# Optimization experiments

Hardware: AMD Instinct MI355X
Metric: run time of the kernel (lower is better)

The kernel has to match this reference:

```python
import jax, jax.numpy as jnp
import numpy as np

NUM_HEADS = 16
MASK_NEG = -66504.0  # matches IPEX causal mask fill value


def setup_inputs() -> dict:
    key = jax.random.key(0)
    ks = jax.random.split(key, 5)
    B, S, E = 1, 2048, 2048
    return {
        "hidden_states": jax.random.normal(ks[0], (B, S, E), dtype=jnp.float32),
        "q_wei": jax.random.normal(ks[1], (E, E), dtype=jnp.float32) * (E ** -0.5),
        "k_wei": jax.random.normal(ks[2], (E, E), dtype=jnp.float32) * (E ** -0.5),
        "v_wei": jax.random.normal(ks[3], (E, E), dtype=jnp.float32) * (E ** -0.5),
        "out_wei": jax.random.normal(ks[4], (E, E), dtype=jnp.float32) * (E ** -0.5),
    }


def reference(hidden_states, q_wei, k_wei, v_wei, out_wei):
    B, S, E = hidden_states.shape
    H = NUM_HEADS
    D = E // H
    # qkv_normal (row-major path): x @ W, [B,S,E]
    q = hidden_states @ q_wei
    k = hidden_states @ k_wei
    v = hidden_states @ v_wei
    # compute_qkv view + normal_combine permute -> [B,H,S,D]
    q = q.reshape(B, S, H, D).transpose(0, 2, 1, 3)
    k = k.reshape(B, S, H, D).transpose(0, 2, 1, 3)
    v = v.reshape(B, S, H, D).transpose(0, 2, 1, 3)
    # naive_self_attention: scores, causal mask add, THEN scale divide
    scores = jnp.einsum("bhqd,bhkd->bhqk", q, k)  # [B,H,S,S]
    causal = jnp.triu(jnp.full((S, S), MASK_NEG, dtype=scores.dtype), k=1)
    scores = scores + causal[None, None]
    scores = scores / jnp.sqrt(jnp.asarray(D, dtype=scores.dtype))
    probs = jax.nn.softmax(scores.astype(jnp.float32), axis=-1).astype(q.dtype)
    attn = jnp.einsum("bhqk,bhkd->bhqd", probs, v)  # [B,H,S,D]
    # merge heads and output projection
    attn = attn.transpose(0, 2, 1, 3).reshape(B, S, E)
    return attn @ out_wei
```

## Files before the change

kernel.cpp:

```cpp
#include <hip/hip_runtime.h>

#define F16 _Float16
typedef __attribute__((ext_vector_type(8))) _Float16 half8;
typedef __attribute__((ext_vector_type(4))) float f32x4;

constexpr int S = 2048;
constexpr int E = 2048;
constexpr float MASK_NEG = -66504.0f;
constexpr float INV_SQRT_D = 0.08838834764831845f;
constexpr float MASK_SC = MASK_NEG * INV_SQRT_D;

__device__ __forceinline__ void gload16(const void* g, void* l) {
  __builtin_amdgcn_global_load_lds((const __attribute__((address_space(1))) void*)g,
                                   (__attribute__((address_space(3))) void*)l, 16, 0, 0);
}

__global__ __launch_bounds__(256) void cast_f32_f16_k(const float* __restrict__ x,
                                                      F16* __restrict__ y) {
  size_t i = ((size_t)blockIdx.x * 256 + threadIdx.x) * 8;
  float4 a = *(const float4*)(x + i);
  float4 b = *(const float4*)(x + i + 4);
  half8 h;
  h[0] = (F16)a.x; h[1] = (F16)a.y; h[2] = (F16)a.z; h[3] = (F16)a.w;
  h[4] = (F16)b.x; h[5] = (F16)b.y; h[6] = (F16)b.z; h[7] = (F16)b.w;
  *(half8*)(y + i) = h;
}

__global__ __launch_bounds__(256) void transpose_cast2_k(const float* __restrict__ W0,
                                                         const float* __restrict__ W1,
                                                         F16* __restrict__ D0,
                                                         F16* __restrict__ D1) {
  const float* W = blockIdx.z ? W1 : W0;
  F16* Wt = blockIdx.z ? D1 : D0;
  __shared__ float tile[64][65];
  const int t = threadIdx.x;
  const int bx = blockIdx.x, by = blockIdx.y;
  {
    int r = t >> 4, c = (t & 15) << 2;
    const float* src = W + (size_t)(by * 64 + r) * E + bx * 64 + c;
    #pragma unroll
    for (int i = 0; i < 4; ++i) {
      float4 v = *(const float4*)(src + (size_t)i * 16 * E);
      tile[r + i * 16][c + 0] = v.x; tile[r + i * 16][c + 1] = v.y;
      tile[r + i * 16][c + 2] = v.z; tile[r + i * 16][c + 3] = v.w;
    }
  }
  __syncthreads();
  {
    int r = t >> 2, c = (t & 3) << 4;
    half8 v0, v1;
    #pragma unroll
    for (int i = 0; i < 8; ++i) v0[i] = (F16)tile[c + i][r];
    #pragma unroll
    for (int i = 0; i < 8; ++i) v1[i] = (F16)tile[c + 8 + i][r];
    F16* dst = Wt + (size_t)(bx * 64 + r) * E + by * 64 + c;
    *(half8*)dst = v0;
    *(half8*)(dst + 8) = v1;
  }
}

template <int MODE>
__global__ __launch_bounds__(256, 2) void gemm_bt_k(const F16* __restrict__ A,
                                                    const F16* __restrict__ Bt,
                                                    void* __restrict__ C0v,
                                                    void* __restrict__ C1v) {
  constexpr int K = 2048, N = 2048;
  __shared__ F16 sA[64 * 64];
  __shared__ F16 sB[128 * 64];
  const int t = threadIdx.x;
  const int lane = t & 63, wave = t >> 6;
  const int wr = wave >> 1, wc = wave & 1;
  const int bm = blockIdx.y, bn = blockIdx.x;

  f32x4 acc[2][4];
  #pragma unroll
  for (int mi = 0; mi < 2; ++mi)
    #pragma unroll
    for (int ni = 0; ni < 4; ++ni) acc[mi][ni] = (f32x4){0.f, 0.f, 0.f, 0.f};

  const int rb = t >> 3;
  const int bofs = (t & 7) << 4;
  const int kOff = (bofs ^ ((rb & 7) << 4)) >> 1;
  const F16* aSrc = A + (size_t)(bm * 64 + rb) * K + kOff;
  const F16* bSrc = Bt + (size_t)(bn * 128 + rb) * K + kOff;
  F16* aDst = sA + t * 8;
  F16* bDst = sB + t * 8;

  for (int bk = 0; bk < K; bk += 64) {
    #pragma unroll
    for (int it = 0; it < 2; ++it)
      gload16(aSrc + (size_t)it * 32 * K + bk, aDst + it * 2048);
    #pragma unroll
    for (int it = 0; it < 4; ++it)
      gload16(bSrc + (size_t)it * 32 * K + bk, bDst + it * 2048);
    __syncthreads();
    #pragma unroll
    for (int kk = 0; kk < 2; ++kk) {
      half8 af[2], bf[4];
      const int kb = kk * 64 + ((lane >> 4) << 4);
      #pragma unroll
      for (int i = 0; i < 2; ++i) {
        const int ra = wr * 32 + i * 16 + (lane & 15);
        af[i] = *(const half8*)((const char*)sA + ra * 128 + (kb ^ ((ra & 7) << 4)));
      }
      #pragma unroll
      for (int i = 0; i < 4; ++i) {
        const int rn = wc * 64 + i * 16 + (lane & 15);
        bf[i] = *(const half8*)((const char*)sB + rn * 128 + (kb ^ ((rn & 7) << 4)));
      }
      #pragma unroll
      for (int mi = 0; mi < 2; ++mi)
        #pragma unroll
        for (int ni = 0; ni < 4; ++ni)
          acc[mi][ni] = __builtin_amdgcn_mfma_f32_16x16x32_f16(af[mi], bf[ni], acc[mi][ni], 0, 0, 0);
    }
    __syncthreads();
  }

  const float scale = (MODE == 1 && bn < 16) ? INV_SQRT_D : 1.0f;
  void* Cv = (MODE == 1 && bn >= 16) ? C1v : C0v;
  const int cb = (MODE == 1 ? (bn & 15) : bn) * 128;

  #pragma unroll
  for (int mi = 0; mi < 2; ++mi) {
    const int r0 = bm * 64 + wr * 32 + mi * 16 + ((lane >> 4) << 2);
    #pragma unroll
    for (int ni = 0; ni < 4; ++ni) {
      const int c = cb + wc * 64 + ni * 16 + (lane & 15);
      #pragma unroll
      for (int j = 0; j < 4; ++j) {
        if (MODE == 2)
          ((float*)Cv)[(size_t)(r0 + j) * N + c] = acc[mi][ni][j];
        else
          ((F16*)Cv)[(size_t)(r0 + j) * N + c] = (F16)(acc[mi][ni][j] * scale);
      }
    }
  }
}

__global__ __launch_bounds__(256, 2) void attn_fwd_k(const F16* __restrict__ Q,
                                                     const F16* __restrict__ Km,
                                                     const F16* __restrict__ Vt,
                                                     F16* __restrict__ O) {
  __shared__ F16 sK[2][64 * 128];
  __shared__ F16 sV[2][128 * 64];
  __shared__ F16 sP[4][16 * 64];
  const int t = threadIdx.x, lane = t & 63, w = t >> 6;
  const int h = blockIdx.x & 15;
  const int bq = blockIdx.x >> 4;
  const int qt = (bq < 16) ? (31 - bq) : (bq - 16);
  const int qrow0 = qt * 64 + w * 16;

  half8 qf[4];
  {
    const int r = qrow0 + (lane & 15);
    const F16* qp = Q + (size_t)r * E + h * 128 + ((lane >> 4) << 3);
    #pragma unroll
    for (int kd = 0; kd < 4; ++kd) qf[kd] = *(const half8*)(qp + kd * 32);
  }

  f32x4 oacc[8];
  #pragma unroll
  for (int i = 0; i < 8; ++i) oacc[i] = (f32x4){0.f, 0.f, 0.f, 0.f};
  float mrow[4] = {-3e38f, -3e38f, -3e38f, -3e38f};
  float lrow[4] = {0.f, 0.f, 0.f, 0.f};

  const int rk = t >> 4;
  const int kcol = (((t & 15) << 4) ^ ((rk & 15) << 4)) >> 1;
  const int rv = t >> 3;
  const int vcol = (((t & 7) << 4) ^ ((rv & 7) << 4)) >> 1;
  const F16* kBase = Km + (size_t)rk * E + h * 128 + kcol;
  const F16* vBase = Vt + (size_t)(h * 128 + rv) * S + vcol;
  F16* myP = (F16*)sP[w];

  auto stage = [&](int kt, int b) {
    const F16* kSrc = kBase + (size_t)kt * 64 * E;
    const F16* vSrc = vBase + kt * 64;
    #pragma unroll
    for (int it = 0; it < 4; ++it) {
      gload16(kSrc + (size_t)it * 16 * E, &sK[b][t * 8 + it * 2048]);
      gload16(vSrc + (size_t)it * 32 * S, &sV[b][t * 8 + it * 2048]);
    }
  };

  stage(0, 0);
  const int nt = qt + 1;

  for (int kt = 0; kt < nt; ++kt) {
    __syncthreads();
    if (kt + 1 < nt) stage(kt + 1, (kt + 1) & 1);
    const char* bK = (const char*)sK[kt & 1];
    const char* bV = (const char*)sV[kt & 1];

    f32x4 sacc[4];
    #pragma unroll
    for (int i = 0; i < 4; ++i) sacc[i] = (f32x4){0.f, 0.f, 0.f, 0.f};
    __builtin_amdgcn_s_setprio(1);
    #pragma unroll
    for (int kd = 0; kd < 4; ++kd) {
      const int kb = kd * 64 + ((lane >> 4) << 4);
      #pragma unroll
      for (int ni = 0; ni < 4; ++ni) {
        const int rn = ni * 16 + (lane & 15);
        half8 bf = *(const half8*)(bK + rn * 256 + (kb ^ ((rn & 15) << 4)));
        sacc[ni] = __builtin_amdgcn_mfma_f32_16x16x32_f16(qf[kd], bf, sacc[ni], 0, 0, 0);
      }
    }
    __builtin_amdgcn_s_setprio(0);

    const bool diag = (kt == nt - 1);
    const int qg0 = qrow0 + ((lane >> 4) << 2);
    const int kg0 = kt * 64 + (lane & 15);
    float mxs[4];
    bool need = false;
    #pragma unroll
    for (int j = 0; j < 4; ++j) {
      float mx = -3e38f;
      #pragma unroll
      for (int ni = 0; ni < 4; ++ni) {
        float s = sacc[ni][j];
        if (diag && (kg0 + ni * 16) > (qg0 + j)) s += MASK_SC;
        sacc[ni][j] = s;
        mx = fmaxf(mx, s);
      }
      mx = fmaxf(mx, __shfl_xor(mx, 1));
      mx = fmaxf(mx, __shfl_xor(mx, 2));
      mx = fmaxf(mx, __shfl_xor(mx, 4));
      mx = fmaxf(mx, __shfl_xor(mx, 8));
      mxs[j] = mx;
      need = need || (mx > mrow[j] + 8.0f);
    }
    if (__any(need)) {
      #pragma unroll
      for (int j = 0; j < 4; ++j) {
        const float mnew = fmaxf(mrow[j], mxs[j]);
        const float sc = __expf(mrow[j] - mnew);
        float rs = 0.f;
        #pragma unroll
        for (int ni = 0; ni < 4; ++ni) {
          const float p = __expf(sacc[ni][j] - mnew);
          sacc[ni][j] = p;
          rs += p;
        }
        rs += __shfl_xor(rs, 1);
        rs += __shfl_xor(rs, 2);
        rs += __shfl_xor(rs, 4);
        rs += __shfl_xor(rs, 8);
        lrow[j] = lrow[j] * sc + rs;
        mrow[j] = mnew;
        #pragma unroll
        for (int df = 0; df < 8; ++df) oacc[df][j] *= sc;
      }
    } else {
      #pragma unroll
      for (int j = 0; j < 4; ++j) {
        float rs = 0.f;
        #pragma unroll
        for (int ni = 0; ni < 4; ++ni) {
          const float p = __expf(sacc[ni][j] - mrow[j]);
          sacc[ni][j] = p;
          rs += p;
        }
        rs += __shfl_xor(rs, 1);
        rs += __shfl_xor(rs, 2);
        rs += __shfl_xor(rs, 4);
        rs += __shfl_xor(rs, 8);
        lrow[j] += rs;
      }
    }

    {
      const int rl0 = (lane >> 4) << 2;
      #pragma unroll
      for (int ni = 0; ni < 4; ++ni) {
        const int cb = (ni * 16 + (lane & 15)) * 2;
        #pragma unroll
        for (int j = 0; j < 4; ++j) {
          const int r = rl0 + j;
          *(F16*)((char*)myP + r * 128 + (cb ^ ((r & 7) << 4))) = (F16)sacc[ni][j];
        }
      }
    }

    __builtin_amdgcn_s_setprio(1);
    #pragma unroll
    for (int kk = 0; kk < 2; ++kk) {
      const int kb = kk * 64 + ((lane >> 4) << 4);
      const int ra = lane & 15;
      half8 pa = *(const half8*)((const char*)myP + ra * 128 + (kb ^ ((ra & 7) << 4)));
      #pragma unroll
      for (int df = 0; df < 8; ++df) {
        const int rd = df * 16 + (lane & 15);
        half8 vf = *(const half8*)(bV + rd * 128 + (kb ^ ((rd & 7) << 4)));
        oacc[df] = __builtin_amdgcn_mfma_f32_16x16x32_f16(pa, vf, oacc[df], 0, 0, 0);
      }
    }
    __builtin_amdgcn_s_setprio(0);
  }

  #pragma unroll
  for (int j = 0; j < 4; ++j) {
    const float inv = 1.0f / lrow[j];
    const int r = qrow0 + ((lane >> 4) << 2) + j;
    F16* op = O + (size_t)r * E + h * 128 + (lane & 15);
    #pragma unroll
    for (int df = 0; df < 8; ++df) op[df * 16] = (F16)(oacc[df][j] * inv);
  }
}

extern "C" void kernel_launch(void* const* d_in, const int* in_sizes, int n_in,
                              void* d_out, int out_size, void* d_ws, size_t ws_size,
                              hipStream_t stream) {
  const float* X  = (const float*)d_in[0];
  const float* Wq = (const float*)d_in[1];
  const float* Wk = (const float*)d_in[2];
  const float* Wv = (const float*)d_in[3];
  const float* Wo = (const float*)d_in[4];
  float* out = (float*)d_out;

  const size_t MAT = (size_t)2048 * 2048;
  F16* Xh  = (F16*)d_ws;
  F16* Wt0 = Xh + MAT;
  F16* Wt1 = Wt0 + MAT;
  F16* Qh  = Wt1 + MAT;
  F16* Kh  = Qh + MAT;
  F16* Vh  = Kh + MAT;

  dim3 b256(256);
  cast_f32_f16_k<<<dim3(MAT / 2048), b256, 0, stream>>>(X, Xh);

  transpose_cast2_k<<<dim3(32, 32, 2), b256, 0, stream>>>(Wq, Wk, Wt0, Wt1);
  gemm_bt_k<1><<<dim3(32, 32), b256, 0, stream>>>(Xh, Wt0, Qh, Kh);

  transpose_cast2_k<<<dim3(32, 32, 2), b256, 0, stream>>>(Wv, Wo, Wt0, Wt1);
  gemm_bt_k<0><<<dim3(16, 32), b256, 0, stream>>>(Wt0, Xh, Vh, nullptr);

  attn_fwd_k<<<dim3(512), b256, 0, stream>>>(Qh, Kh, Vh, Xh);

  gemm_bt_k<2><<<dim3(16, 32), b256, 0, stream>>>(Xh, Wt1, out, nullptr);
}
```

Before: 195.1 us.

## Transpose attention MFMA operands so each lane owns one query row

Swaps the A/B operands of both MFMAs in the attention kernel so that S^T and O^T accumulate with each lane holding a single query row. Softmax max and sum reductions drop from four 4-step shuffles per row to two shuffles across lane groups, and running max/sum collapse to one scalar per lane. P is written to shared memory as packed half4 instead of scalar halves, and output stores become half4 vectors. This reduces shuffle and scalar LDS/global store overhead, but changes the register layout and the masking index math.

```diff
diff --git a/kernel.cpp b/kernel.cpp
--- a/kernel.cpp
+++ b/kernel.cpp
@@ -2,6 +2,7 @@
 
 #define F16 _Float16
 typedef __attribute__((ext_vector_type(8))) _Float16 half8;
+typedef __attribute__((ext_vector_type(4))) _Float16 half4;
 typedef __attribute__((ext_vector_type(4))) float f32x4;
 
 constexpr int S = 2048;
@@ -150,11 +151,12 @@
   const int bq = blockIdx.x >> 4;
   const int qt = (bq < 16) ? (31 - bq) : (bq - 16);
   const int qrow0 = qt * 64 + w * 16;
+  const int g = lane >> 4;
+  const int myq = qrow0 + (lane & 15);
 
   half8 qf[4];
   {
-    const int r = qrow0 + (lane & 15);
-    const F16* qp = Q + (size_t)r * E + h * 128 + ((lane >> 4) << 3);
+    const F16* qp = Q + (size_t)myq * E + h * 128 + (g << 3);
     #pragma unroll
     for (int kd = 0; kd < 4; ++kd) qf[kd] = *(const half8*)(qp + kd * 32);
   }
@@ -162,8 +164,7 @@
   f32x4 oacc[8];
   #pragma unroll
   for (int i = 0; i < 8; ++i) oacc[i] = (f32x4){0.f, 0.f, 0.f, 0.f};
-  float mrow[4] = {-3e38f, -3e38f, -3e38f, -3e38f};
-  float lrow[4] = {0.f, 0.f, 0.f, 0.f};
+  float mrun = -3e38f, lrun = 0.f;
 
   const int rk = t >> 4;
   const int kcol = (((t & 15) << 4) ^ ((rk & 15) << 4)) >> 1;
@@ -198,113 +199,103 @@
     __builtin_amdgcn_s_setprio(1);
     #pragma unroll
     for (int kd = 0; kd < 4; ++kd) {
-      const int kb = kd * 64 + ((lane >> 4) << 4);
+      const int kb = kd * 64 + (g << 4);
       #pragma unroll
       for (int ni = 0; ni < 4; ++ni) {
         const int rn = ni * 16 + (lane & 15);
-        half8 bf = *(const half8*)(bK + rn * 256 + (kb ^ ((rn & 15) << 4)));
-        sacc[ni] = __builtin_amdgcn_mfma_f32_16x16x32_f16(qf[kd], bf, sacc[ni], 0, 0, 0);
+        half8 kf = *(const half8*)(bK + rn * 256 + (kb ^ ((rn & 15) << 4)));
+        sacc[ni] = __builtin_amdgcn_mfma_f32_16x16x32_f16(kf, qf[kd], sacc[ni], 0, 0, 0);
       }
     }
     __builtin_amdgcn_s_setprio(0);
 
     const bool diag = (kt == nt - 1);
-    const int qg0 = qrow0 + ((lane >> 4) << 2);
-    const int kg0 = kt * 64 + (lane & 15);
-    float mxs[4];
-    bool need = false;
-    #pragma unroll
-    for (int j = 0; j < 4; ++j) {
-      float mx = -3e38f;
-      #pragma unroll
-      for (int ni = 0; ni < 4; ++ni) {
+    const int kv0 = kt * 64 + g * 4;
+    float mx = -3e38f;
+    #pragma unroll
+    for (int ni = 0; ni < 4; ++ni) {
+      #pragma unroll
+      for (int j = 0; j < 4; ++j) {
         float s = sacc[ni][j];
-        if (diag && (kg0 + ni * 16) > (qg0 + j)) s += MASK_SC;
+        if (diag && (kv0 + ni * 16 + j) > myq) s += MASK_SC;
         sacc[ni][j] = s;
         mx = fmaxf(mx, s);
       }
-      mx = fmaxf(mx, __shfl_xor(mx, 1));
-      mx = fmaxf(mx, __shfl_xor(mx, 2));
-      mx = fmaxf(mx, __shfl_xor(mx, 4));
-      mx = fmaxf(mx, __shfl_xor(mx, 8));
-      mxs[j] = mx;
-      need = need || (mx > mrow[j] + 8.0f);
-    }
-    if (__any(need)) {
-      #pragma unroll
-      for (int j = 0; j < 4; ++j) {
-        const float mnew = fmaxf(mrow[j], mxs[j]);
-        const float sc = __expf(mrow[j] - mnew);
-        float rs = 0.f;
-        #pragma unroll
-        for (int ni = 0; ni < 4; ++ni) {
+    }
+    mx = fmaxf(mx, __shfl_xor(mx, 16));
+    mx = fmaxf(mx, __shfl_xor(mx, 32));
+
+    if (__any(mx > mrun + 8.0f)) {
+      const float mnew = fmaxf(mrun, mx);
+      const float sc = __expf(mrun - mnew);
+      float rs = 0.f;
+      #pragma unroll
+      for (int ni = 0; ni < 4; ++ni)
+        #pragma unroll
+        for (int j = 0; j < 4; ++j) {
           const float p = __expf(sacc[ni][j] - mnew);
           sacc[ni][j] = p;
           rs += p;
         }
-        rs += __shfl_xor(rs, 1);
-        rs += __shfl_xor(rs, 2);
-        rs += __shfl_xor(rs, 4);
-        rs += __shfl_xor(rs, 8);
-        lrow[j] = lrow[j] * sc + rs;
-        mrow[j] = mnew;
-        #pragma unroll
-        for (int df = 0; df < 8; ++df) oacc[df][j] *= sc;
-      }
+      rs += __shfl_xor(rs, 16);
+      rs += __shfl_xor(rs, 32);
+      lrun = lrun * sc + rs;
+      mrun = mnew;
+      #pragma unroll
+      for (int df = 0; df < 8; ++df)
+        #pragma unroll
+        for (int j = 0; j < 4; ++j) oacc[df][j] *= sc;
     } else {
-      #pragma unroll
-      for (int j = 0; j < 4; ++j) {
-        float rs = 0.f;
-        #pragma unroll
-        for (int ni = 0; ni < 4; ++ni) {
-          const float p = __expf(sacc[ni][j] - mrow[j]);
+      float rs = 0.f;
+      #pragma unroll
+      for (int ni = 0; ni < 4; ++ni)
+        #pragma unroll
+        for (int j = 0; j < 4; ++j) {
+          const float p = __expf(sacc[ni][j] - mrun);
           sacc[ni][j] = p;
           rs += p;
         }
-        rs += __shfl_xor(rs, 1);
-        rs += __shfl_xor(rs, 2);
-        rs += __shfl_xor(rs, 4);
-        rs += __shfl_xor(rs, 8);
-        lrow[j] += rs;
-      }
+      rs += __shfl_xor(rs, 16);
+      rs += __shfl_xor(rs, 32);
+      lrun += rs;
     }
 
     {
-      const int rl0 = (lane >> 4) << 2;
+      char* rowp = (char*)myP + (lane & 15) * 128;
+      const int swz = ((lane & 15) & 7) << 4;
       #pragma unroll
       for (int ni = 0; ni < 4; ++ni) {
-        const int cb = (ni * 16 + (lane & 15)) * 2;
-        #pragma unroll
-        for (int j = 0; j < 4; ++j) {
-          const int r = rl0 + j;
-          *(F16*)((char*)myP + r * 128 + (cb ^ ((r & 7) << 4))) = (F16)sacc[ni][j];
-        }
+        half4 pk;
+        #pragma unroll
+        for (int j = 0; j < 4; ++j) pk[j] = (F16)sacc[ni][j];
+        *(half4*)(rowp + ((ni * 32 + g * 8) ^ swz)) = pk;
       }
     }
 
     __builtin_amdgcn_s_setprio(1);
     #pragma unroll
     for (int kk = 0; kk < 2; ++kk) {
-      const int kb = kk * 64 + ((lane >> 4) << 4);
+      const int kb = kk * 64 + (g << 4);
       const int ra = lane & 15;
       half8 pa = *(const half8*)((const char*)myP + ra * 128 + (kb ^ ((ra & 7) << 4)));
       #pragma unroll
       for (int df = 0; df < 8; ++df) {
         const int rd = df * 16 + (lane & 15);
         half8 vf = *(const half8*)(bV + rd * 128 + (kb ^ ((rd & 7) << 4)));
-        oacc[df] = __builtin_amdgcn_mfma_f32_16x16x32_f16(pa, vf, oacc[df], 0, 0, 0);
+        oacc[df] = __builtin_amdgcn_mfma_f32_16x16x32_f16(vf, pa, oacc[df], 0, 0, 0);
       }
     }
     __builtin_amdgcn_s_setprio(0);
   }
 
+  const float inv = 1.0f / lrun;
+  F16* orow = O + (size_t)myq * E + h * 128;
   #pragma unroll
-  for (int j = 0; j < 4; ++j) {
-    const float inv = 1.0f / lrow[j];
-    const int r = qrow0 + ((lane >> 4) << 2) + j;
-    F16* op = O + (size_t)r * E + h * 128 + (lane & 15);
-    #pragma unroll
-    for (int df = 0; df < 8; ++df) op[df * 16] = (F16)(oacc[df][j] * inv);
+  for (int df = 0; df < 8; ++df) {
+    half4 ov;
+    #pragma unroll
+    for (int j = 0; j < 4; ++j) ov[j] = (F16)(oacc[df][j] * inv);
+    *(half4*)(orow + df * 16 + g * 4) = ov;
   }
 }
 
```

Result: faster. 178.9 us (-8.3%).
